# Performance work log

Measured on AMD Instinct MI355X. Metric: run time of the kernel, lower is better.

Reference implementation:

```python
import math
import jax, jax.numpy as jnp
import numpy as np

G_RATIO = 0.5
TB_FACTOR = 1e-3


def _expand(x):
    # x: [B,H,W]; 3x3 all-ones-except-center neighbor conv (same filter for every sample)
    k = jnp.ones((1, 1, 3, 3), x.dtype).at[0, 0, 1, 1].set(0.0)
    y = jax.lax.conv_general_dilated(x[:, None], k, (1, 1), 'SAME')
    return y[:, 0]


def _st_softmax_noexp(val):
    # straight-through normalized selection over flattened map
    B = val.shape[0]
    v = val.reshape(B, -1)
    y = v / v.sum(-1, keepdims=True)
    ind = jnp.argmax(y, -1)
    y_hard = jax.nn.one_hot(ind, y.shape[-1], dtype=y.dtype)
    y = y + jax.lax.stop_gradient(y_hard - y)
    return y.reshape(val.shape)


def _heuristic(gm):
    # gm: [B,H,W] one-hot goal maps -> Chebyshev + tb*Euclidean distance field
    B, H, W = gm.shape
    loc = jnp.stack(jnp.meshgrid(jnp.arange(H), jnp.arange(W), indexing='ij'), 0).astype(gm.dtype)  # [2,H,W]
    loc_e = loc.reshape(2, -1)[None]                      # [1,2,HW]
    goal_loc = jnp.einsum('kij,bij->bk', loc, gm)[:, :, None]  # [B,2,1]
    d = jnp.abs(loc_e - goal_loc)                         # [B,2,HW]
    h = d.sum(1) - d.min(1)
    euc = jnp.sqrt(((loc_e - goal_loc) ** 2).sum(1))
    return (h + TB_FACTOR * euc).reshape(B, H, W)


def _forward_core(cost_maps, start_maps, goal_maps, obstacles_maps):
    cm, sm, gm, om = cost_maps[:, 0], start_maps[:, 0], goal_maps[:, 0], obstacles_maps[:, 0]
    B, H, W = cm.shape
    h = _heuristic(gm) + cm
    goal_idx = jnp.argmax(gm.reshape(B, -1), -1)
    parents0 = jnp.broadcast_to(goal_idx[:, None].astype(cm.dtype), (B, H * W))
    inv_sqrt = 1.0 / math.sqrt(W)
    Tmax = W * W

    def step(carry, i):
        g, open_m, hist, parents, done, t = carry
        f = G_RATIO * g + (1.0 - G_RATIO) * h
        f_exp = jnp.exp(-f * inv_sqrt) * open_m
        snm = _st_softmax_noexp(f_exp)
        dist = (snm * gm).sum((1, 2), keepdims=True)
        unsolved = (dist < 1e-8).astype(cm.dtype)
        hist_n = jnp.clip(hist + snm, 0.0, 1.0)
        open_n = jnp.clip(open_m - unsolved * snm, 0.0, 1.0)
        nb = _expand(snm) * om
        g2 = _expand((g + cm) * snm)
        idx = ((1.0 - open_n) * (1.0 - hist_n) + open_n * (g > g2).astype(cm.dtype)) * nb
        idx = jax.lax.stop_gradient(idx)
        g_n = jax.lax.stop_gradient(g2 * idx + g * (1.0 - idx))
        open_n = jax.lax.stop_gradient(jnp.clip(open_n + idx, 0.0, 1.0))
        idx_f = idx.reshape(B, -1)
        new_par = jnp.argmax(snm.reshape(B, -1), -1)[:, None].astype(cm.dtype)
        par_n = new_par * idx_f + parents * (1.0 - idx_f)
        done_n = jnp.all(unsolved == 0)
        sel = lambda new, old: jnp.where(done, old, new)  # emulate the torch early break
        carry_n = (sel(g_n, g), sel(open_n, open_m), sel(hist_n, hist), sel(par_n, parents),
                   jnp.logical_or(done, done_n), jnp.where(done, t, i))
        return carry_n, None

    init = (jnp.zeros_like(sm), sm, jnp.zeros_like(sm), parents0,
            jnp.array(False), jnp.array(0, jnp.int32))
    (g, open_m, hist, parents, done, t), _ = jax.lax.scan(
        step, init, jnp.arange(Tmax, dtype=jnp.int32))
    return hist[:, None], parents, t


def _backtrack(goal_maps, parents, t):
    gm = goal_maps[:, 0]
    B, H, W = gm.shape
    par_i = parents.astype(jnp.int32)
    goal_f = gm.reshape(B, -1).astype(jnp.int32)
    loc = (par_i * goal_f).sum(-1)
    rng = jnp.arange(B)

    def bt(i, val):
        path, loc = val
        path = path.at[rng, loc].set(1)
        loc = jnp.take_along_axis(par_i, loc[:, None], -1)[:, 0]
        return (path, loc)

    path, _ = jax.lax.fori_loop(0, t, bt, (goal_f, loc))
    return path.reshape(B, 1, H, W)


def setup_inputs() -> dict:
    key = jax.random.key(0)
    k1, k2, k3, k4 = jax.random.split(key, 4)
    B, H, W = 16, 32, 32
    cost_maps = jax.random.uniform(k1, (B, 1, H, W), dtype=jnp.float32)
    sidx = jax.random.randint(k2, (B,), 0, H * W)
    gidx = jax.random.randint(k3, (B,), 0, H * W)
    gidx = jnp.where(gidx == sidx, (gidx + 1) % (H * W), gidx)
    start_maps = jax.nn.one_hot(sidx, H * W, dtype=jnp.float32).reshape(B, 1, H, W)
    goal_maps = jax.nn.one_hot(gidx, H * W, dtype=jnp.float32).reshape(B, 1, H, W)
    obstacles_maps = (jax.random.uniform(k4, (B, 1, H, W)) > 0.05).astype(jnp.float32)
    obstacles_maps = jnp.clip(obstacles_maps + start_maps + goal_maps, 0.0, 1.0)
    return {'cost_maps': cost_maps, 'start_maps': start_maps,
            'goal_maps': goal_maps, 'obstacles_maps': obstacles_maps}


def reference(cost_maps, start_maps, goal_maps, obstacles_maps):
    histories, parents, t = _forward_core(cost_maps, start_maps, goal_maps, obstacles_maps)
    path_maps = _backtrack(goal_maps, parents, t)
    return histories, path_maps
```

## Files before the change

kernel.cpp:

```cpp
#include <hip/hip_runtime.h>
#include <math.h>

#define HW 1024
#define NB 16
#define TMAXS 1024

typedef unsigned long long ull;

__device__ __forceinline__ double u2d(ull u) {
  return __longlong_as_double((long long)u);
}
__device__ __forceinline__ ull d2u(double d) {
  return (ull)__double_as_longlong(d);
}

__device__ __forceinline__ float keyhalf(float gh, float hh) {
#pragma clang fp contract(off)
  const float INV = 0.17677669529663687f;
  return expf(-(gh + hh) * INV);
}

__device__ __forceinline__ ull packkey(float keyf, int idx) {
  return ((ull)__float_as_uint(keyf) << 32) | (ull)(1023 - idx);
}

template <int CTRL>
__device__ __forceinline__ double dpp_fmax64(double x) {
  ull u = d2u(x);
  int lo = (int)(unsigned)u;
  int hi = (int)(unsigned)(u >> 32);
  int lo2 = __builtin_amdgcn_update_dpp(0, lo, CTRL, 0xF, 0xF, false);
  int hi2 = __builtin_amdgcn_update_dpp(0, hi, CTRL, 0xF, 0xF, false);
  double y = u2d(((ull)(unsigned)hi2 << 32) | (unsigned)lo2);
  return fmax(x, y);
}

__device__ __forceinline__ ull rdl64(double d, int l) {
  ull u = d2u(d);
  int lo = __builtin_amdgcn_readlane((int)(unsigned)u, l);
  int hi = __builtin_amdgcn_readlane((int)(unsigned)(u >> 32), l);
  return ((ull)(unsigned)hi << 32) | (unsigned)lo;
}

extern "C" __global__ void __launch_bounds__(64) astar_fused(
    const float* __restrict__ cm_g, const float* __restrict__ sm_g,
    const float* __restrict__ gm_g, const float* __restrict__ om_g,
    float* __restrict__ out) {
#pragma clang fp contract(off)
  const int b = blockIdx.x;
  const int lane = threadIdx.x;

  __shared__ __align__(16) uint4 cellT[HW];
  __shared__ __align__(16) ull key2[HW];
  __shared__ __align__(16) unsigned par[HW];
  __shared__ __align__(16) ull level1[64];
  const float2* cell2 = (const float2*)cellT;
  unsigned* cellu = (unsigned*)cellT;

  const float* cm = cm_g + b * HW;
  const float* sm = sm_g + b * HW;
  const float* gm = gm_g + b * HW;
  const float* om = om_g + b * HW;

  float4 c4[4], o4[4];
  int gi = -1, si = -1;
#pragma unroll
  for (int q = 0; q < 4; ++q) {
    const int base = q * 256 + lane * 4;
    c4[q] = *(const float4*)(cm + base);
    o4[q] = *(const float4*)(om + base);
    const float4 s4 = *(const float4*)(sm + base);
    const float4 g4 = *(const float4*)(gm + base);
    const float sv[4] = {s4.x, s4.y, s4.z, s4.w};
    const float gv[4] = {g4.x, g4.y, g4.z, g4.w};
#pragma unroll
    for (int j = 0; j < 4; ++j) {
      if (gv[j] > 0.5f) gi = base + j;
      if (sv[j] > 0.5f) si = base + j;
    }
  }
#pragma unroll
  for (int m = 32; m >= 1; m >>= 1) {
    const int og = __shfl_xor(gi, m, 64);
    const int os = __shfl_xor(si, m, 64);
    gi = (og > gi) ? og : gi;
    si = (os > si) ? os : si;
  }
  const int goal = __builtin_amdgcn_readfirstlane(gi);
  const int start = __builtin_amdgcn_readfirstlane(si);

  level1[lane] = 0ull;
  const float grf = (float)(goal >> 5), gcf = (float)(goal & 31);
#pragma unroll
  for (int q = 0; q < 4; ++q) {
    const int base = q * 256 + lane * 4;
    const float cv[4] = {c4[q].x, c4[q].y, c4[q].z, c4[q].w};
    const float ov[4] = {o4[q].x, o4[q].y, o4[q].z, o4[q].w};
    ull pk[4];
#pragma unroll
    for (int j = 0; j < 4; ++j) {
      const int cell = base + j;
      const float rr = (float)(cell >> 5), cc = (float)(cell & 31);
      const float dr = fabsf(rr - grf), dc = fabsf(cc - gcf);
      const float h0 = (dr + dc) - fminf(dr, dc);
      const float euc = sqrtf(dr * dr + dc * dc);
      const float t1 = 0.001f * euc;
      const float hh = h0 + t1;
      const float hf = hh + cv[j];
      const float hw = 0.5f * hf;
      unsigned fv = (ov[j] > 0.5f) ? 1u : 0u;
      pk[j] = (ull)(1023 - cell);
      if (cell == start) {
        fv |= 2u;
        pk[j] = packkey(keyhalf(0.0f, hw), cell);
      }
      cellT[cell] = make_uint4(__float_as_uint(0.0f), __float_as_uint(cv[j]),
                               __float_as_uint(hw), fv);
      atomicMax(&level1[cell >> 4], pk[j]);
    }
    *(uint4*)&par[base] =
        make_uint4((unsigned)goal, (unsigned)goal, (unsigned)goal, (unsigned)goal);
    ulonglong2 k01, k23;
    k01.x = pk[0]; k01.y = pk[1];
    k23.x = pk[2]; k23.y = pk[3];
    *(ulonglong2*)&key2[base] = k01;
    *(ulonglong2*)&key2[base + 2] = k23;
  }
  __builtin_amdgcn_wave_barrier();
  ull stale = level1[lane];

  int dlt = 0;
  if (lane < 8) {
    const int k = (lane < 4) ? lane : lane + 1;
    dlt = (k / 3 - 1) * 32 + (k % 3 - 1);
  }

  int sel = start;
  bool reached = false;

#pragma unroll 1
  for (int step = 0; step < TMAXS; ++step) {
    if (sel == goal) { reached = true; break; }
    const int gp = sel >> 4;

    const int sr = sel >> 5, sc = sel & 31;
    unsigned vmask = 0xFFu;
    if (sr == 0) vmask &= ~0x07u;
    if (sr == 31) vmask &= ~0xE0u;
    if (sc == 0) vmask &= ~0x29u;
    if (sc == 31) vmask &= ~0x94u;

    const float2 sg = cell2[2 * sel];
    const int n = sel + dlt;
    const bool relaxer = (lane < 8) && ((vmask >> lane) & 1u);
    uint4 nv = make_uint4(0u, 0u, 0u, 0u);
    if (relaxer) nv = cellT[n];
    const bool gcl = (lane >= 16) && (lane < 32);
    const int gcell = gp * 16 + (lane - 16);
    ull gco = 0ull;
    if (gcl) gco = key2[gcell];

    double ma = (lane == gp) ? 0.0 : u2d(stale);
    ma = dpp_fmax64<0x111>(ma);
    ma = dpp_fmax64<0x112>(ma);
    ma = dpp_fmax64<0x114>(ma);
    ma = dpp_fmax64<0x118>(ma);
    ma = dpp_fmax64<0x142>(ma);
    ma = dpp_fmax64<0x143>(ma);

    const float g2full = sg.x + sg.y;
    const float g2h = 0.5f * g2full;
    const unsigned f = nv.w;
    const bool updv =
        relaxer && (f & 1u) &&
        (((f & 6u) == 0u) || (((f & 2u) != 0u) && (__uint_as_float(nv.x) > g2full)));
    if (updv) {
      cellT[n] = make_uint4(__float_as_uint(g2full), nv.y, nv.z, f | 2u);
      par[n] = (unsigned)sel;
    }
    if (lane == 8) {
      cellu[4 * sel + 3] = 5u;
      key2[sel] = (ull)(1023 - sel);
    }

    ull gcp = gco;
    if (gcl && gcell == sel) gcp = (ull)(1023 - sel);
    double mc = gcl ? u2d(gcp) : 0.0;
    mc = dpp_fmax64<0x111>(mc);
    mc = dpp_fmax64<0x112>(mc);
    mc = dpp_fmax64<0x114>(mc);
    mc = dpp_fmax64<0x118>(mc);
    if (lane == 31) level1[gp] = d2u(mc);

    const ull GC = rdl64(mc, 31);
    const ull MA = rdl64(ma, 63);
    const ull MACv = (GC > MA) ? GC : MA;

    ull pk = 0ull;
    if (updv) pk = packkey(keyhalf(g2h, __uint_as_float(nv.z)), n);
    if (updv) key2[n] = pk;
    if (updv) atomicMax(&level1[n >> 4], pk);
    const ull stale_n = level1[lane];

    double mb = updv ? u2d(pk) : 0.0;
    mb = dpp_fmax64<0x111>(mb);
    mb = dpp_fmax64<0x112>(mb);
    mb = dpp_fmax64<0x114>(mb);
    const ull PB = rdl64(mb, 7);

    const ull M = (PB > MACv) ? PB : MACv;
    sel = 1023 - (int)((unsigned)M & 1023u);
    stale = stale_n;
    __builtin_amdgcn_wave_barrier();
  }
  if (reached && lane == 0) cellu[4 * goal + 3] |= 4u;
  __builtin_amdgcn_wave_barrier();

  if (lane == 0) {
    const unsigned pv = par[goal];
    par[goal] = pv | 0x80000000u;
    unsigned loc = pv & 1023u;
#pragma unroll 1
    for (int i = 0; i < HW; ++i) {
      const unsigned w = par[loc];
      if (w & 0x80000000u) break;
      par[loc] = w | 0x80000000u;
      loc = w & 1023u;
    }
  }
  __builtin_amdgcn_wave_barrier();

#pragma unroll
  for (int q = 0; q < 4; ++q) {
    const int base = q * 256 + lane * 4;
    float4 hv, pv;
    hv.x = (cellu[4 * (base + 0) + 3] & 4u) ? 1.0f : 0.0f;
    hv.y = (cellu[4 * (base + 1) + 3] & 4u) ? 1.0f : 0.0f;
    hv.z = (cellu[4 * (base + 2) + 3] & 4u) ? 1.0f : 0.0f;
    hv.w = (cellu[4 * (base + 3) + 3] & 4u) ? 1.0f : 0.0f;
    pv.x = (par[base + 0] >> 31) ? 1.0f : 0.0f;
    pv.y = (par[base + 1] >> 31) ? 1.0f : 0.0f;
    pv.z = (par[base + 2] >> 31) ? 1.0f : 0.0f;
    pv.w = (par[base + 3] >> 31) ? 1.0f : 0.0f;
    *(float4*)(out + b * HW + base) = hv;
    *(float4*)(out + NB * HW + b * HW + base) = pv;
  }
}

extern "C" void kernel_launch(void* const* d_in, const int* in_sizes, int n_in,
                              void* d_out, int out_size, void* d_ws,
                              size_t ws_size, hipStream_t stream) {
  const float* cm = (const float*)d_in[0];
  const float* sm = (const float*)d_in[1];
  const float* gm = (const float*)d_in[2];
  const float* om = (const float*)d_in[3];
  float* out = (float*)d_out;
  hipLaunchKernelGGL(astar_fused, dim3(NB), dim3(64), 0, stream, cm, sm, gm,
                     om, out);
}
```

Measured before the change: 79.35 us.

## Precompute neighbor priority keys one step ahead across all 64 lanes

Adds a per-cell table of eight candidate exp keys that is filled speculatively for each neighbor updated in the previous step, using all 64 lanes (8 neighbors x 8 second-hop neighbors). This takes the expf off the serial critical path between selecting a cell and publishing its neighbors' keys. The cost is 32 KB more LDS, extra LDS reads and writes every step, and key computations that are often wasted.

```diff
diff --git a/kernel.cpp b/kernel.cpp
--- a/kernel.cpp
+++ b/kernel.cpp
@@ -18,10 +18,6 @@
 #pragma clang fp contract(off)
   const float INV = 0.17677669529663687f;
   return expf(-(gh + hh) * INV);
-}
-
-__device__ __forceinline__ ull packkey(float keyf, int idx) {
-  return ((ull)__float_as_uint(keyf) << 32) | (ull)(1023 - idx);
 }
 
 template <int CTRL>
@@ -42,6 +38,21 @@
   return ((ull)(unsigned)hi << 32) | (unsigned)lo;
 }
 
+__device__ __forceinline__ int dlt_of(int idx) {
+  const int k = (idx < 4) ? idx : idx + 1;
+  return (k / 3 - 1) * 32 + (k % 3 - 1);
+}
+
+__device__ __forceinline__ unsigned vmask_of(int cell) {
+  unsigned m = 0xFFu;
+  const int r = cell >> 5, c = cell & 31;
+  if (r == 0) m &= ~0x07u;
+  if (r == 31) m &= ~0xE0u;
+  if (c == 0) m &= ~0x29u;
+  if (c == 31) m &= ~0x94u;
+  return m;
+}
+
 extern "C" __global__ void __launch_bounds__(64) astar_fused(
     const float* __restrict__ cm_g, const float* __restrict__ sm_g,
     const float* __restrict__ gm_g, const float* __restrict__ om_g,
@@ -54,6 +65,7 @@
   __shared__ __align__(16) ull key2[HW];
   __shared__ __align__(16) unsigned par[HW];
   __shared__ __align__(16) ull level1[64];
+  __shared__ __align__(16) unsigned pkeys[HW * 8];
   const float2* cell2 = (const float2*)cellT;
   unsigned* cellu = (unsigned*)cellT;
 
@@ -90,6 +102,10 @@
   const int start = __builtin_amdgcn_readfirstlane(si);
 
   level1[lane] = 0ull;
+#pragma unroll
+  for (int q = 0; q < 32; ++q) {
+    *(uint4*)&pkeys[q * 256 + lane * 4] = make_uint4(0u, 0u, 0u, 0u);
+  }
   const float grf = (float)(goal >> 5), gcf = (float)(goal & 31);
 #pragma unroll
   for (int q = 0; q < 4; ++q) {
@@ -112,7 +128,8 @@
       pk[j] = (ull)(1023 - cell);
       if (cell == start) {
         fv |= 2u;
-        pk[j] = packkey(keyhalf(0.0f, hw), cell);
+        pk[j] = ((ull)__float_as_uint(keyhalf(0.0f, hw)) << 32) |
+                (ull)(1023 - cell);
       }
       cellT[cell] = make_uint4(__float_as_uint(0.0f), __float_as_uint(cv[j]),
                                __float_as_uint(hw), fv);
@@ -127,13 +144,25 @@
     *(ulonglong2*)&key2[base + 2] = k23;
   }
   __builtin_amdgcn_wave_barrier();
+
+  {
+    const float cs = __uint_as_float(cellu[4 * start + 1]);
+    if (lane < 8) {
+      const int m = (start + dlt_of(lane)) & 1023;
+      const float hwm = __uint_as_float(cellu[4 * m + 2]);
+      const float s0 = 0.0f + cs;
+      const float gh0 = 0.5f * s0;
+      const unsigned vm = vmask_of(start);
+      if ((vm >> lane) & 1u)
+        pkeys[start * 8 + lane] = __float_as_uint(keyhalf(gh0, hwm));
+    }
+  }
+  __builtin_amdgcn_wave_barrier();
   ull stale = level1[lane];
 
-  int dlt = 0;
-  if (lane < 8) {
-    const int k = (lane < 4) ? lane : lane + 1;
-    dlt = (k / 3 - 1) * 32 + (k % 3 - 1);
-  }
+  const int dltrl = dlt_of(lane & 7);
+  const int dltjj = dlt_of(lane >> 3);
+  const int rl = lane & 7;
 
   int sel = start;
   bool reached = false;
@@ -142,23 +171,23 @@
   for (int step = 0; step < TMAXS; ++step) {
     if (sel == goal) { reached = true; break; }
     const int gp = sel >> 4;
-
-    const int sr = sel >> 5, sc = sel & 31;
-    unsigned vmask = 0xFFu;
-    if (sr == 0) vmask &= ~0x07u;
-    if (sr == 31) vmask &= ~0xE0u;
-    if (sc == 0) vmask &= ~0x29u;
-    if (sc == 31) vmask &= ~0x94u;
+    const unsigned vmask = vmask_of(sel);
 
     const float2 sg = cell2[2 * sel];
-    const int n = sel + dlt;
+    const int n = sel + dltrl;
     const bool relaxer = (lane < 8) && ((vmask >> lane) & 1u);
     uint4 nv = make_uint4(0u, 0u, 0u, 0u);
     if (relaxer) nv = cellT[n];
+    unsigned pkb = 0u;
+    if (lane < 8) pkb = pkeys[sel * 8 + lane];
     const bool gcl = (lane >= 16) && (lane < 32);
     const int gcell = gp * 16 + (lane - 16);
     ull gco = 0ull;
     if (gcl) gco = key2[gcell];
+    const int nrlc = (sel + dltrl) & 1023;
+    const int mfk = (nrlc + dltjj) & 1023;
+    const float cm8 = __uint_as_float(cellu[4 * nrlc + 1]);
+    const float hw8 = __uint_as_float(cellu[4 * mfk + 2]);
 
     double ma = (lane == gp) ? 0.0 : u2d(stale);
     ma = dpp_fmax64<0x111>(ma);
@@ -169,7 +198,6 @@
     ma = dpp_fmax64<0x143>(ma);
 
     const float g2full = sg.x + sg.y;
-    const float g2h = 0.5f * g2full;
     const unsigned f = nv.w;
     const bool updv =
         relaxer && (f & 1u) &&
@@ -197,7 +225,7 @@
     const ull MACv = (GC > MA) ? GC : MA;
 
     ull pk = 0ull;
-    if (updv) pk = packkey(keyhalf(g2h, __uint_as_float(nv.z)), n);
+    if (updv) pk = ((ull)pkb << 32) | (ull)(1023 - n);
     if (updv) key2[n] = pk;
     if (updv) atomicMax(&level1[n >> 4], pk);
     const ull stale_n = level1[lane];
@@ -209,7 +237,16 @@
     const ull PB = rdl64(mb, 7);
 
     const ull M = (PB > MACv) ? PB : MACv;
-    sel = 1023 - (int)((unsigned)M & 1023u);
+    const int nsel = 1023 - (int)((unsigned)M & 1023u);
+
+    const ull bal = __ballot(updv);
+    if ((bal >> rl) & 1ull) {
+      const float sfk = g2full + cm8;
+      const float ghfk = 0.5f * sfk;
+      pkeys[nrlc * 8 + (lane >> 3)] = __float_as_uint(keyhalf(ghfk, hw8));
+    }
+
+    sel = nsel;
     stale = stale_n;
     __builtin_amdgcn_wave_barrier();
   }
```

Result: no change. 80.67 us (+1.7%).
